# Optimization experiments

Measured on AMD Instinct MI355X. Metric: run time of the kernel, lower is better.

The kernel has to match this reference:

```python
import jax, jax.numpy as jnp
import numpy as np

V, E, H = 50000, 100, 128
B, S = 16, 4096
NUM_LEVELS = int(np.log2(S)) + 1  # 13; level l has S >> l nodes
# gate order in the 5-gate stack: i, f_l, f_r, o, u
XMAP = jnp.array([0, 1, 1, 2, 3])


def setup_inputs() -> dict:
    key = jax.random.key(0)
    ks = jax.random.split(key, 9)
    sE = 1.0 / np.sqrt(E)
    sH = 1.0 / np.sqrt(H)
    return {
        "embedding": jax.random.normal(ks[0], (V, E), jnp.float32) * 0.1,
        "W_x": jax.random.normal(ks[1], (4, H, E), jnp.float32) * sE,   # (i,f,o,u) x-projections
        "b_x": jax.random.normal(ks[2], (4, H), jnp.float32) * sE,
        "U_l": jax.random.normal(ks[3], (5, H, H), jnp.float32) * sH,   # (u_i_l,u_f_ll,u_f_rr,u_o_l,u_u_l) applied to h_left
        "b_l": jax.random.normal(ks[4], (5, H), jnp.float32) * sH,
        "U_r": jax.random.normal(ks[5], (5, H, H), jnp.float32) * sH,   # (u_i_r,u_f_lr,u_f_rl,u_o_r,u_u_r) applied to h_right
        "b_r": jax.random.normal(ks[6], (5, H), jnp.float32) * sH,
        "input_seq": jax.random.randint(ks[7], (B, S), 0, V, jnp.int32),
        "dep_tags": jax.random.randint(ks[8], (NUM_LEVELS - 1, S // 2), 0, S, jnp.int32),
    }


def _level_step(x5, h_l, h_r, c_l, c_r, U_l, b_l, U_r, b_r):
    # x5: [B,N,5,H] per-gate x contributions (w_*(x) incl. bias)
    pre = (x5
           + jnp.einsum('bnk,ghk->bngh', h_l, U_l) + b_l
           + jnp.einsum('bnk,ghk->bngh', h_r, U_r) + b_r)  # [B,N,5,H]
    i   = jax.nn.sigmoid(pre[:, :, 0])
    f_l = jax.nn.sigmoid(pre[:, :, 1])
    f_r = jax.nn.sigmoid(pre[:, :, 2])
    o   = jax.nn.sigmoid(pre[:, :, 3])
    u   = jnp.tanh(pre[:, :, 4])
    c = i * u + f_l * c_l + f_r * c_r
    h = o * jnp.tanh(c)
    return h, c


def reference(embedding, W_x, b_x, U_l, b_l, U_r, b_r, input_seq, dep_tags):
    b, s = input_seq.shape
    emb = embedding[input_seq]  # [B,S,E]
    xg = jnp.einsum('bse,ghe->bsgh', emb, W_x) + b_x  # [B,S,4,H]

    # level 0: every leaf is a token, children are zero
    z = jnp.zeros((b, s, xg.shape[-1]), xg.dtype)
    h, c = _level_step(xg[:, :, XMAP, :], z, z, z, z, U_l, b_l, U_r, b_r)

    for l in range(1, NUM_LEVELS):
        n = s >> l
        dep = dep_tags[l - 1, :n]                # token position re-embedded at each internal node
        x5 = xg[:, dep][:, :, XMAP, :]           # [B,N,5,H]
        hp = h.reshape(b, n, 2, -1)              # node i's children are (2i, 2i+1)
        cp = c.reshape(b, n, 2, -1)
        h, c = _level_step(x5, hp[:, :, 0], hp[:, :, 1], cp[:, :, 0], cp[:, :, 1],
                           U_l, b_l, U_r, b_r)
    return h[:, 0], c[:, 0]  # root (h, c): [B,H] each
```

## Files before the change

### kernel.cpp

```cpp
#include <hip/hip_runtime.h>
#include <hip/hip_bf16.h>

#define V_ 50000
#define E_ 100
#define H_ 128
#define B_ 16
#define S_ 4096

typedef unsigned short u16;
typedef unsigned int   u32;
typedef short bf16x8 __attribute__((ext_vector_type(8)));
typedef float f32x4  __attribute__((ext_vector_type(4)));

__device__ __forceinline__ float bf2f(u16 x) {
  return __uint_as_float(((u32)x) << 16);
}
__device__ __forceinline__ u16 f2bf(float x) {
  __hip_bfloat16 b = __float2bfloat16(x);
  return *reinterpret_cast<u16*>(&b);
}
__device__ __forceinline__ float sigm(float x) { return 1.0f / (1.0f + __expf(-x)); }
__device__ __forceinline__ float tanh_f(float x) {
  float e = __expf(2.0f * x);
  return 1.0f - 2.0f / (e + 1.0f);
}

#define PREP_N0 (V_ * 128)
#define PREP_N1 65536
#define PREP_N2 163840
#define PREP_N3 640
__global__ __launch_bounds__(256) void prep_all(
    const float* __restrict__ emb, const float* __restrict__ Wx,
    const float* __restrict__ Ul, const float* __restrict__ Ur,
    const float* __restrict__ bl, const float* __restrict__ br,
    u16* __restrict__ embB, u16* __restrict__ Bx, u16* __restrict__ Bu,
    float* __restrict__ bs)
{
  int i = blockIdx.x * 256 + threadIdx.x;
  if (i < PREP_N0) {
    int k = i & 127, t = i >> 7;
    embB[i] = (k < E_) ? f2bf(emb[t * E_ + k]) : (u16)0;
    return;
  }
  i -= PREP_N0;
  if (i < PREP_N1) {
    int j = i & 7, l = (i >> 3) & 63, s = (i >> 9) & 3, t = i >> 11;
    int k = s * 32 + (l >> 4) * 8 + j;
    int o = t * 16 + (l & 15);
    Bx[i] = (k < E_) ? f2bf(Wx[o * E_ + k]) : (u16)0;
    return;
  }
  i -= PREP_N1;
  if (i < PREP_N2) {
    int j = i & 7, l = (i >> 3) & 63, s = (i >> 9) & 7, t = i >> 12;
    int k = s * 32 + (l >> 4) * 8 + j;
    int gh = t * 16 + (l & 15);
    float v = (k < 128) ? Ul[gh * 128 + k] : Ur[gh * 128 + (k - 128)];
    Bu[i] = f2bf(v);
    return;
  }
  i -= PREP_N2;
  if (i < PREP_N3) bs[i] = bl[i] + br[i];
}

#define XLDS 516
__global__ __launch_bounds__(512) void xg_mfma(
    const u16* __restrict__ embB, const u16* __restrict__ Bx,
    const float* __restrict__ bx, const int* __restrict__ seq,
    const float* __restrict__ bs,
    ushort4* __restrict__ xg, u16* __restrict__ h0, float* __restrict__ c0)
{
  __shared__ u16 lds[32 * XLDS];
  const int w = threadIdx.x >> 6, lane = threadIdx.x & 63;
  const int quad = lane >> 4, l15 = lane & 15;
  const int m0 = blockIdx.x * 32;

  f32x4 acc[2][4];
  #pragma unroll
  for (int r = 0; r < 2; ++r)
    #pragma unroll
    for (int t = 0; t < 4; ++t) acc[r][t] = (f32x4){0.f, 0.f, 0.f, 0.f};

  int tok0 = seq[m0 + l15];
  int tok1 = seq[m0 + 16 + l15];
  const u16* a0p = embB + (size_t)tok0 * 128 + quad * 8;
  const u16* a1p = embB + (size_t)tok1 * 128 + quad * 8;

  #pragma unroll
  for (int s = 0; s < 4; ++s) {
    bf16x8 a0 = *reinterpret_cast<const bf16x8*>(a0p + s * 32);
    bf16x8 a1 = *reinterpret_cast<const bf16x8*>(a1p + s * 32);
    #pragma unroll
    for (int ti = 0; ti < 4; ++ti) {
      int t = w * 4 + ti;
      bf16x8 b = *reinterpret_cast<const bf16x8*>(Bx + ((size_t)(t * 4 + s) * 64 + lane) * 8);
      acc[0][ti] = __builtin_amdgcn_mfma_f32_16x16x32_bf16(a0, b, acc[0][ti], 0, 0, 0);
      acc[1][ti] = __builtin_amdgcn_mfma_f32_16x16x32_bf16(a1, b, acc[1][ti], 0, 0, 0);
    }
  }

  const int g = w >> 1;
  #pragma unroll
  for (int ti = 0; ti < 4; ++ti) {
    int o = (w * 4 + ti) * 16 + l15;
    float bxo = bx[o];
    int hhw = (w & 1) * 64 + ti * 16 + l15;
    #pragma unroll
    for (int r = 0; r < 2; ++r)
      #pragma unroll
      for (int reg = 0; reg < 4; ++reg) {
        int mrow = r * 16 + quad * 4 + reg;
        lds[mrow * XLDS + hhw * 4 + g] = f2bf(acc[r][ti][reg] + bxo);
      }
  }
  __syncthreads();

  #pragma unroll
  for (int i = 0; i < 8; ++i) {
    int pidx = i * 512 + threadIdx.x;
    int m = pidx >> 7, hh = pidx & 127;
    ushort4 v = *reinterpret_cast<const ushort4*>(&lds[m * XLDS + hh * 4]);
    size_t gm = (size_t)(m0 + m);
    xg[gm * 128 + hh] = v;
    float pi = bf2f(v.x) + bs[hh];
    float po = bf2f(v.z) + bs[384 + hh];
    float pu = bf2f(v.w) + bs[512 + hh];
    float c = sigm(pi) * tanh_f(pu);
    float h = sigm(po) * tanh_f(c);
    h0[gm * 128 + hh] = f2bf(h);
    c0[gm * 128 + hh] = c;
  }
}

__global__ __launch_bounds__(512) void level_mfma64(
    const ushort4* __restrict__ xg4, const int* __restrict__ deprow,
    const u16* __restrict__ Bu, const float* __restrict__ bs,
    const u16* __restrict__ hPrev, const float* __restrict__ cPrev,
    u16* __restrict__ hOut, float* __restrict__ cOut, int n, int ln2n)
{
  const int w = threadIdx.x >> 6, lane = threadIdx.x & 63;
  const int quad = lane >> 4, l15 = lane & 15;
  const int hh = w * 16 + l15;
  const int m0 = blockIdx.x * 64;

  ushort4 xv[16];
  #pragma unroll
  for (int i = 0; i < 16; ++i) {
    int m = m0 + (i >> 2) * 16 + quad * 4 + (i & 3);
    int j = m & (n - 1);
    int b = m >> ln2n;
    xv[i] = xg4[((size_t)b * S_ + deprow[j]) * 128 + hh];
  }

  f32x4 acc[4][5];
  #pragma unroll
  for (int r = 0; r < 4; ++r)
    #pragma unroll
    for (int g = 0; g < 5; ++g) acc[r][g] = (f32x4){0.f, 0.f, 0.f, 0.f};

  const u16* ap = hPrev + (size_t)(m0 + l15) * 256 + quad * 8;

  #pragma unroll
  for (int s = 0; s < 8; ++s) {
    bf16x8 a[4];
    #pragma unroll
    for (int r = 0; r < 4; ++r)
      a[r] = *reinterpret_cast<const bf16x8*>(ap + (size_t)r * 16 * 256 + s * 32);
    #pragma unroll
    for (int g = 0; g < 5; ++g) {
      int t = g * 8 + w;
      bf16x8 b = *reinterpret_cast<const bf16x8*>(Bu + ((size_t)(t * 8 + s) * 64 + lane) * 8);
      #pragma unroll
      for (int r = 0; r < 4; ++r)
        acc[r][g] = __builtin_amdgcn_mfma_f32_16x16x32_bf16(a[r], b, acc[r][g], 0, 0, 0);
    }
  }

  float bsv[5];
  #pragma unroll
  for (int g = 0; g < 5; ++g) bsv[g] = bs[g * 128 + hh];

  #pragma unroll
  for (int i = 0; i < 16; ++i) {
    int r = i >> 2, reg = i & 3;
    int m = m0 + r * 16 + quad * 4 + reg;
    ushort4 v = xv[i];
    float x0 = bf2f(v.x), x1 = bf2f(v.y), x2 = bf2f(v.z), x3 = bf2f(v.w);
    float cl = cPrev[(size_t)m * 256 + hh];
    float cr = cPrev[(size_t)m * 256 + 128 + hh];
    float pi  = acc[r][0][reg] + x0 + bsv[0];
    float pfl = acc[r][1][reg] + x1 + bsv[1];
    float pfr = acc[r][2][reg] + x1 + bsv[2];
    float po  = acc[r][3][reg] + x2 + bsv[3];
    float pu  = acc[r][4][reg] + x3 + bsv[4];
    float c = sigm(pi) * tanh_f(pu) + sigm(pfl) * cl + sigm(pfr) * cr;
    float h = sigm(po) * tanh_f(c);
    hOut[(size_t)m * 128 + hh] = f2bf(h);
    cOut[(size_t)m * 128 + hh] = c;
  }
}

__global__ __launch_bounds__(512) void level_mfma(
    const ushort4* __restrict__ xg4, const int* __restrict__ deprow,
    const u16* __restrict__ Bu, const float* __restrict__ bs,
    const u16* __restrict__ hPrev, const float* __restrict__ cPrev,
    u16* __restrict__ hOut, float* __restrict__ cOut, int n, int ln2n)
{
  const int w = threadIdx.x >> 6, lane = threadIdx.x & 63;
  const int quad = lane >> 4, l15 = lane & 15;
  const int hh = w * 16 + l15;
  const int m0 = blockIdx.x * 32;

  ushort4 xv[8];
  float clv[8], crv[8];
  #pragma unroll
  for (int i = 0; i < 8; ++i) {
    int m = m0 + (i >> 2) * 16 + quad * 4 + (i & 3);
    int j = m & (n - 1);
    int b = m >> ln2n;
    int dj = deprow[j];
    xv[i] = xg4[((size_t)b * S_ + dj) * 128 + hh];
    clv[i] = cPrev[(size_t)m * 256 + hh];
    crv[i] = cPrev[(size_t)m * 256 + 128 + hh];
  }

  f32x4 acc[2][5];
  #pragma unroll
  for (int r = 0; r < 2; ++r)
    #pragma unroll
    for (int g = 0; g < 5; ++g) acc[r][g] = (f32x4){0.f, 0.f, 0.f, 0.f};

  const u16* a0p = hPrev + (size_t)(m0 + l15) * 256 + quad * 8;
  const u16* a1p = a0p + 16 * 256;

  #pragma unroll
  for (int s = 0; s < 8; ++s) {
    bf16x8 a0 = *reinterpret_cast<const bf16x8*>(a0p + s * 32);
    bf16x8 a1 = *reinterpret_cast<const bf16x8*>(a1p + s * 32);
    #pragma unroll
    for (int g = 0; g < 5; ++g) {
      int t = g * 8 + w;
      bf16x8 b = *reinterpret_cast<const bf16x8*>(Bu + ((size_t)(t * 8 + s) * 64 + lane) * 8);
      acc[0][g] = __builtin_amdgcn_mfma_f32_16x16x32_bf16(a0, b, acc[0][g], 0, 0, 0);
      acc[1][g] = __builtin_amdgcn_mfma_f32_16x16x32_bf16(a1, b, acc[1][g], 0, 0, 0);
    }
  }

  float bsv[5];
  #pragma unroll
  for (int g = 0; g < 5; ++g) bsv[g] = bs[g * 128 + hh];

  #pragma unroll
  for (int i = 0; i < 8; ++i) {
    int r = i >> 2, reg = i & 3;
    int m = m0 + r * 16 + quad * 4 + reg;
    ushort4 v = xv[i];
    float x0 = bf2f(v.x), x1 = bf2f(v.y), x2 = bf2f(v.z), x3 = bf2f(v.w);
    float pi  = acc[r][0][reg] + x0 + bsv[0];
    float pfl = acc[r][1][reg] + x1 + bsv[1];
    float pfr = acc[r][2][reg] + x1 + bsv[2];
    float po  = acc[r][3][reg] + x2 + bsv[3];
    float pu  = acc[r][4][reg] + x3 + bsv[4];
    float c = sigm(pi) * tanh_f(pu) + sigm(pfl) * clv[i] + sigm(pfr) * crv[i];
    float h = sigm(po) * tanh_f(c);
    hOut[(size_t)m * 128 + hh] = f2bf(h);
    cOut[(size_t)m * 128 + hh] = c;
  }
}

__global__ __launch_bounds__(512) void deep_fused(
    const ushort4* __restrict__ xg4, const int* __restrict__ dep,
    const u16* __restrict__ Bu, const float* __restrict__ bs,
    const u16* __restrict__ h6, const float* __restrict__ c6,
    float* __restrict__ out)
{
  __shared__ u16  hls[2][32 * 136];
  __shared__ float cls[2][32 * 128];
  const int b = blockIdx.x;
  const int w = threadIdx.x >> 6, lane = threadIdx.x & 63;
  const int quad = lane >> 4, l15 = lane & 15;
  const int hh = w * 16 + l15;

  float bsv[5];
  #pragma unroll
  for (int g = 0; g < 5; ++g) bsv[g] = bs[g * 128 + hh];

  {
    ushort4 xv[2][4];
    float clv[2][4], crv[2][4];
    #pragma unroll
    for (int r = 0; r < 2; ++r)
      #pragma unroll
      for (int reg = 0; reg < 4; ++reg) {
        int j = r * 16 + quad * 4 + reg;
        int dj = dep[6 * 2048 + j];
        xv[r][reg] = xg4[((size_t)b * S_ + dj) * 128 + hh];
        clv[r][reg] = c6[(size_t)(b * 32 + j) * 256 + hh];
        crv[r][reg] = c6[(size_t)(b * 32 + j) * 256 + 128 + hh];
      }

    f32x4 acc[2][5];
    #pragma unroll
    for (int r = 0; r < 2; ++r)
      #pragma unroll
      for (int g = 0; g < 5; ++g) acc[r][g] = (f32x4){0.f, 0.f, 0.f, 0.f};

    #pragma unroll
    for (int s = 0; s < 8; ++s) {
      const u16* ap = h6 + (size_t)(b * 32 + l15) * 256 + s * 32 + quad * 8;
      bf16x8 a0 = *reinterpret_cast<const bf16x8*>(ap);
      bf16x8 a1 = *reinterpret_cast<const bf16x8*>(ap + 16 * 256);
      #pragma unroll
      for (int g = 0; g < 5; ++g) {
        int t = g * 8 + w;
        bf16x8 bb = *reinterpret_cast<const bf16x8*>(Bu + ((size_t)(t * 8 + s) * 64 + lane) * 8);
        acc[0][g] = __builtin_amdgcn_mfma_f32_16x16x32_bf16(a0, bb, acc[0][g], 0, 0, 0);
        acc[1][g] = __builtin_amdgcn_mfma_f32_16x16x32_bf16(a1, bb, acc[1][g], 0, 0, 0);
      }
    }

    #pragma unroll
    for (int r = 0; r < 2; ++r)
      #pragma unroll
      for (int reg = 0; reg < 4; ++reg) {
        int j = r * 16 + quad * 4 + reg;
        ushort4 v = xv[r][reg];
        float x0 = bf2f(v.x), x1 = bf2f(v.y), x2 = bf2f(v.z), x3 = bf2f(v.w);
        float pi  = acc[r][0][reg] + x0 + bsv[0];
        float pfl = acc[r][1][reg] + x1 + bsv[1];
        float pfr = acc[r][2][reg] + x1 + bsv[2];
        float po  = acc[r][3][reg] + x2 + bsv[3];
        float pu  = acc[r][4][reg] + x3 + bsv[4];
        float c = sigm(pi) * tanh_f(pu) + sigm(pfl) * clv[r][reg] + sigm(pfr) * crv[r][reg];
        float h = sigm(po) * tanh_f(c);
        hls[0][j * 136 + hh] = f2bf(h);
        cls[0][j * 128 + hh] = c;
      }
  }
  __syncthreads();

  ushort4 xvc[4];
  #pragma unroll
  for (int reg = 0; reg < 4; ++reg)
    xvc[reg] = xg4[((size_t)b * S_ + dep[7 * 2048 + quad * 4 + reg]) * 128 + hh];

  int pb = 0;
  for (int lvl = 8; lvl <= 12; ++lvl) {
    int nb = 4096 >> lvl;

    ushort4 xvn[4];
    if (lvl < 12) {
      int nbn = 2048 >> lvl;
      #pragma unroll
      for (int reg = 0; reg < 4; ++reg) {
        int j = quad * 4 + reg;
        if (j < nbn)
          xvn[reg] = xg4[((size_t)b * S_ + dep[lvl * 2048 + j]) * 128 + hh];
      }
    }

    f32x4 acc[5];
    #pragma unroll
    for (int g = 0; g < 5; ++g) acc[g] = (f32x4){0.f, 0.f, 0.f, 0.f};

    #pragma unroll
    for (int s = 0; s < 8; ++s) {
      int child = 2 * l15 + (s >= 4 ? 1 : 0);
      int kk = (s & 3) * 32 + quad * 8;
      bf16x8 a = *reinterpret_cast<const bf16x8*>(&hls[pb][child * 136 + kk]);
      #pragma unroll
      for (int g = 0; g < 5; ++g) {
        int t = g * 8 + w;
        bf16x8 bb = *reinterpret_cast<const bf16x8*>(Bu + ((size_t)(t * 8 + s) * 64 + lane) * 8);
        acc[g] = __builtin_amdgcn_mfma_f32_16x16x32_bf16(a, bb, acc[g], 0, 0, 0);
      }
    }

    #pragma unroll
    for (int reg = 0; reg < 4; ++reg) {
      int j = quad * 4 + reg;
      if (j < nb) {
        ushort4 v = xvc[reg];
        float x0 = bf2f(v.x), x1 = bf2f(v.y), x2 = bf2f(v.z), x3 = bf2f(v.w);
        float cl = cls[pb][(2 * j) * 128 + hh];
        float cr = cls[pb][(2 * j + 1) * 128 + hh];
        float pi  = acc[0][reg] + x0 + bsv[0];
        float pfl = acc[1][reg] + x1 + bsv[1];
        float pfr = acc[2][reg] + x1 + bsv[2];
        float po  = acc[3][reg] + x2 + bsv[3];
        float pu  = acc[4][reg] + x3 + bsv[4];
        float c = sigm(pi) * tanh_f(pu) + sigm(pfl) * cl + sigm(pfr) * cr;
        float h = sigm(po) * tanh_f(c);
        hls[pb ^ 1][j * 136 + hh] = f2bf(h);
        cls[pb ^ 1][j * 128 + hh] = c;
        if (lvl == 12) {
          out[b * 128 + hh] = h;
          out[2048 + b * 128 + hh] = c;
        }
      }
    }
    __syncthreads();
    pb ^= 1;
    #pragma unroll
    for (int reg = 0; reg < 4; ++reg) xvc[reg] = xvn[reg];
  }
}

extern "C" void kernel_launch(void* const* d_in, const int* in_sizes, int n_in,
                              void* d_out, int out_size, void* d_ws, size_t ws_size,
                              hipStream_t stream)
{
  const float* emb = (const float*)d_in[0];
  const float* Wx  = (const float*)d_in[1];
  const float* bx  = (const float*)d_in[2];
  const float* Ul  = (const float*)d_in[3];
  const float* bl  = (const float*)d_in[4];
  const float* Ur  = (const float*)d_in[5];
  const float* br  = (const float*)d_in[6];
  const int* seq = (const int*)d_in[7];
  const int* dep = (const int*)d_in[8];

  char* p = (char*)d_ws;
  u16* embB = (u16*)p;   p += (size_t)V_ * 128 * 2;
  u16* BswX = (u16*)p;   p += 131072;
  u16* BswU = (u16*)p;   p += 327680;
  float* bs = (float*)p; p += 4096;
  u16* xg = (u16*)p;     p += (size_t)B_ * S_ * 512 * 2;
  u16* hA = (u16*)p;     p += (size_t)B_ * S_ * H_ * 2;
  float* cA = (float*)p; p += (size_t)B_ * S_ * H_ * 4;
  u16* hB = (u16*)p;     p += (size_t)B_ * (S_ / 2) * H_ * 2;
  float* cB = (float*)p; p += (size_t)B_ * (S_ / 2) * H_ * 4;

  const int prep_tot = PREP_N0 + PREP_N1 + PREP_N2 + PREP_N3;
  prep_all<<<dim3((prep_tot + 255) / 256), dim3(256), 0, stream>>>(
      emb, Wx, Ul, Ur, bl, br, embB, BswX, BswU, bs);

  xg_mfma<<<dim3(B_ * S_ / 32), dim3(512), 0, stream>>>(
      embB, BswX, bx, seq, bs, (ushort4*)xg, hA, cA);

  const ushort4* xg4 = (const ushort4*)xg;
  u16 *hp = hA, *ho = hB;
  float *cp = cA, *co = cB;
  for (int l = 1; l <= 3; ++l) {
    int n = S_ >> l;
    int Mtot = B_ * n;
    const int* deprow = dep + (size_t)(l - 1) * (S_ / 2);
    level_mfma64<<<dim3(Mtot / 64), dim3(512), 0, stream>>>(
        xg4, deprow, BswU, bs, hp, cp, ho, co, n, 12 - l);
    u16* th = hp; hp = ho; ho = th;
    float* tc = cp; cp = co; co = tc;
  }
  for (int l = 4; l <= 6; ++l) {
    int n = S_ >> l;
    int Mtot = B_ * n;
    const int* deprow = dep + (size_t)(l - 1) * (S_ / 2);
    level_mfma<<<dim3(Mtot / 32), dim3(512), 0, stream>>>(
        xg4, deprow, BswU, bs, hp, cp, ho, co, n, 12 - l);
    u16* th = hp; hp = ho; ho = th;
    float* tc = cp; cp = co; co = tc;
  }

  deep_fused<<<dim3(16), dim3(512), 0, stream>>>(
      xg4, dep, BswU, bs, hp, cp, (float*)d_out);
}
```

Baseline: 271.0 us.

## Fuse level-0 leaf cell into level-1 kernel and fold biases into xg

```diff
diff --git a/kernel.cpp b/kernel.cpp
--- a/kernel.cpp
+++ b/kernel.cpp
@@ -33,8 +33,9 @@
     const float* __restrict__ emb, const float* __restrict__ Wx,
     const float* __restrict__ Ul, const float* __restrict__ Ur,
     const float* __restrict__ bl, const float* __restrict__ br,
+    const float* __restrict__ bx,
     u16* __restrict__ embB, u16* __restrict__ Bx, u16* __restrict__ Bu,
-    float* __restrict__ bs)
+    float* __restrict__ bxs, float* __restrict__ bd)
 {
   int i = blockIdx.x * 256 + threadIdx.x;
   if (i < PREP_N0) {
@@ -60,15 +61,21 @@
     return;
   }
   i -= PREP_N2;
-  if (i < PREP_N3) bs[i] = bl[i] + br[i];
-}
-
-#define XLDS 516
+  if (i < 512) {
+    int g = i >> 7, hh = i & 127;
+    int lg = (g == 0) ? 0 : (g == 1) ? 1 : (g == 2) ? 3 : 4;
+    bxs[i] = bx[i] + bl[lg * 128 + hh] + br[lg * 128 + hh];
+    return;
+  }
+  i -= 512;
+  if (i < 128) bd[i] = (bl[256 + i] + br[256 + i]) - (bl[128 + i] + br[128 + i]);
+}
+
+#define XLDS 514
 __global__ __launch_bounds__(512) void xg_mfma(
     const u16* __restrict__ embB, const u16* __restrict__ Bx,
-    const float* __restrict__ bx, const int* __restrict__ seq,
-    const float* __restrict__ bs,
-    ushort4* __restrict__ xg, u16* __restrict__ h0, float* __restrict__ c0)
+    const float* __restrict__ bxs, const int* __restrict__ seq,
+    ushort4* __restrict__ xg)
 {
   __shared__ u16 lds[32 * XLDS];
   const int w = threadIdx.x >> 6, lane = threadIdx.x & 63;
@@ -103,7 +110,7 @@
   #pragma unroll
   for (int ti = 0; ti < 4; ++ti) {
     int o = (w * 4 + ti) * 16 + l15;
-    float bxo = bx[o];
+    float bxo = bxs[o];
     int hhw = (w & 1) * 64 + ti * 16 + l15;
     #pragma unroll
     for (int r = 0; r < 2; ++r)
@@ -120,21 +127,97 @@
     int pidx = i * 512 + threadIdx.x;
     int m = pidx >> 7, hh = pidx & 127;
     ushort4 v = *reinterpret_cast<const ushort4*>(&lds[m * XLDS + hh * 4]);
-    size_t gm = (size_t)(m0 + m);
-    xg[gm * 128 + hh] = v;
-    float pi = bf2f(v.x) + bs[hh];
-    float po = bf2f(v.z) + bs[384 + hh];
-    float pu = bf2f(v.w) + bs[512 + hh];
-    float c = sigm(pi) * tanh_f(pu);
+    xg[(size_t)(m0 + m) * 128 + hh] = v;
+  }
+}
+
+__global__ __launch_bounds__(512) void level1_mfma(
+    const ushort4* __restrict__ xg4, const int* __restrict__ deprow,
+    const u16* __restrict__ Bu, const float* __restrict__ bd,
+    u16* __restrict__ hOut, float* __restrict__ cOut)
+{
+  const int w = threadIdx.x >> 6, lane = threadIdx.x & 63;
+  const int quad = lane >> 4, l15 = lane & 15;
+  const int hh = w * 16 + l15;
+  const int m0 = blockIdx.x * 32;
+
+  ushort4 xv[8];
+  #pragma unroll
+  for (int i = 0; i < 8; ++i) {
+    int m = m0 + (i >> 2) * 16 + quad * 4 + (i & 3);
+    int j = m & 2047;
+    int b = m >> 11;
+    xv[i] = xg4[((size_t)b * S_ + deprow[j]) * 128 + hh];
+  }
+
+  f32x4 acc[2][5];
+  #pragma unroll
+  for (int r = 0; r < 2; ++r)
+    #pragma unroll
+    for (int g = 0; g < 5; ++g) acc[r][g] = (f32x4){0.f, 0.f, 0.f, 0.f};
+
+  #pragma unroll
+  for (int s = 0; s < 8; ++s) {
+    bf16x8 a[2];
+    #pragma unroll
+    for (int r = 0; r < 2; ++r) {
+      int row2 = 2 * (m0 + r * 16 + l15) + (s >> 2);
+      const uint4* xp = reinterpret_cast<const uint4*>(
+          xg4 + (size_t)row2 * 128 + (s & 3) * 32 + quad * 8);
+      #pragma unroll
+      for (int jj = 0; jj < 4; ++jj) {
+        uint4 q = xp[jj];
+        {
+          float pi = __uint_as_float(q.x << 16);
+          float po = __uint_as_float(q.y << 16);
+          float pu = __uint_as_float(q.y & 0xffff0000u);
+          float c = sigm(pi) * tanh_f(pu);
+          a[r][2 * jj] = (short)f2bf(sigm(po) * tanh_f(c));
+        }
+        {
+          float pi = __uint_as_float(q.z << 16);
+          float po = __uint_as_float(q.w << 16);
+          float pu = __uint_as_float(q.w & 0xffff0000u);
+          float c = sigm(pi) * tanh_f(pu);
+          a[r][2 * jj + 1] = (short)f2bf(sigm(po) * tanh_f(c));
+        }
+      }
+    }
+    #pragma unroll
+    for (int g = 0; g < 5; ++g) {
+      int t = g * 8 + w;
+      bf16x8 b = *reinterpret_cast<const bf16x8*>(Bu + ((size_t)(t * 8 + s) * 64 + lane) * 8);
+      acc[0][g] = __builtin_amdgcn_mfma_f32_16x16x32_bf16(a[0], b, acc[0][g], 0, 0, 0);
+      acc[1][g] = __builtin_amdgcn_mfma_f32_16x16x32_bf16(a[1], b, acc[1][g], 0, 0, 0);
+    }
+  }
+
+  float bdv = bd[hh];
+  #pragma unroll
+  for (int i = 0; i < 8; ++i) {
+    int r = i >> 2, reg = i & 3;
+    int m = m0 + r * 16 + quad * 4 + reg;
+    ushort4 vl = xg4[(size_t)(2 * m) * 128 + hh];
+    ushort4 vr = xg4[(size_t)(2 * m + 1) * 128 + hh];
+    float cl = sigm(bf2f(vl.x)) * tanh_f(bf2f(vl.w));
+    float cr = sigm(bf2f(vr.x)) * tanh_f(bf2f(vr.w));
+    ushort4 v = xv[i];
+    float x0 = bf2f(v.x), x1 = bf2f(v.y), x2 = bf2f(v.z), x3 = bf2f(v.w);
+    float pi  = acc[r][0][reg] + x0;
+    float pfl = acc[r][1][reg] + x1;
+    float pfr = acc[r][2][reg] + x1 + bdv;
+    float po  = acc[r][3][reg] + x2;
+    float pu  = acc[r][4][reg] + x3;
+    float c = sigm(pi) * tanh_f(pu) + sigm(pfl) * cl + sigm(pfr) * cr;
     float h = sigm(po) * tanh_f(c);
-    h0[gm * 128 + hh] = f2bf(h);
-    c0[gm * 128 + hh] = c;
+    hOut[(size_t)m * 128 + hh] = f2bf(h);
+    cOut[(size_t)m * 128 + hh] = c;
   }
 }
 
 __global__ __launch_bounds__(512) void level_mfma64(
     const ushort4* __restrict__ xg4, const int* __restrict__ deprow,
-    const u16* __restrict__ Bu, const float* __restrict__ bs,
+    const u16* __restrict__ Bu, const float* __restrict__ bd,
     const u16* __restrict__ hPrev, const float* __restrict__ cPrev,
     u16* __restrict__ hOut, float* __restrict__ cOut, int n, int ln2n)
 {
@@ -176,10 +259,7 @@
     }
   }
 
-  float bsv[5];
-  #pragma unroll
-  for (int g = 0; g < 5; ++g) bsv[g] = bs[g * 128 + hh];
-
+  float bdv = bd[hh];
   #pragma unroll
   for (int i = 0; i < 16; ++i) {
     int r = i >> 2, reg = i & 3;
@@ -188,11 +268,11 @@
     float x0 = bf2f(v.x), x1 = bf2f(v.y), x2 = bf2f(v.z), x3 = bf2f(v.w);
     float cl = cPrev[(size_t)m * 256 + hh];
     float cr = cPrev[(size_t)m * 256 + 128 + hh];
-    float pi  = acc[r][0][reg] + x0 + bsv[0];
-    float pfl = acc[r][1][reg] + x1 + bsv[1];
-    float pfr = acc[r][2][reg] + x1 + bsv[2];
-    float po  = acc[r][3][reg] + x2 + bsv[3];
-    float pu  = acc[r][4][reg] + x3 + bsv[4];
+    float pi  = acc[r][0][reg] + x0;
+    float pfl = acc[r][1][reg] + x1;
+    float pfr = acc[r][2][reg] + x1 + bdv;
+    float po  = acc[r][3][reg] + x2;
+    float pu  = acc[r][4][reg] + x3;
     float c = sigm(pi) * tanh_f(pu) + sigm(pfl) * cl + sigm(pfr) * cr;
     float h = sigm(po) * tanh_f(c);
     hOut[(size_t)m * 128 + hh] = f2bf(h);
@@ -202,7 +282,7 @@
 
 __global__ __launch_bounds__(512) void level_mfma(
     const ushort4* __restrict__ xg4, const int* __restrict__ deprow,
-    const u16* __restrict__ Bu, const float* __restrict__ bs,
+    const u16* __restrict__ Bu, const float* __restrict__ bd,
     const u16* __restrict__ hPrev, const float* __restrict__ cPrev,
     u16* __restrict__ hOut, float* __restrict__ cOut, int n, int ln2n)
 {
@@ -246,21 +326,18 @@
     }
   }
 
-  float bsv[5];
-  #pragma unroll
-  for (int g = 0; g < 5; ++g) bsv[g] = bs[g * 128 + hh];
-
+  float bdv = bd[hh];
   #pragma unroll
   for (int i = 0; i < 8; ++i) {
     int r = i >> 2, reg = i & 3;
     int m = m0 + r * 16 + quad * 4 + reg;
     ushort4 v = xv[i];
     float x0 = bf2f(v.x), x1 = bf2f(v.y), x2 = bf2f(v.z), x3 = bf2f(v.w);
-    float pi  = acc[r][0][reg] + x0 + bsv[0];
-    float pfl = acc[r][1][reg] + x1 + bsv[1];
-    float pfr = acc[r][2][reg] + x1 + bsv[2];
-    float po  = acc[r][3][reg] + x2 + bsv[3];
-    float pu  = acc[r][4][reg] + x3 + bsv[4];
+    float pi  = acc[r][0][reg] + x0;
+    float pfl = acc[r][1][reg] + x1;
+    float pfr = acc[r][2][reg] + x1 + bdv;
+    float po  = acc[r][3][reg] + x2;
+    float pu  = acc[r][4][reg] + x3;
     float c = sigm(pi) * tanh_f(pu) + sigm(pfl) * clv[i] + sigm(pfr) * crv[i];
     float h = sigm(po) * tanh_f(c);
     hOut[(size_t)m * 128 + hh] = f2bf(h);
@@ -270,7 +347,7 @@
 
 __global__ __launch_bounds__(512) void deep_fused(
     const ushort4* __restrict__ xg4, const int* __restrict__ dep,
-    const u16* __restrict__ Bu, const float* __restrict__ bs,
+    const u16* __restrict__ Bu, const float* __restrict__ bd,
     const u16* __restrict__ h6, const float* __restrict__ c6,
     float* __restrict__ out)
 {
@@ -281,9 +358,7 @@
   const int quad = lane >> 4, l15 = lane & 15;
   const int hh = w * 16 + l15;
 
-  float bsv[5];
-  #pragma unroll
-  for (int g = 0; g < 5; ++g) bsv[g] = bs[g * 128 + hh];
+  const float bdv = bd[hh];
 
   {
     ushort4 xv[2][4];
@@ -326,11 +401,11 @@
         int j = r * 16 + quad * 4 + reg;
         ushort4 v = xv[r][reg];
         float x0 = bf2f(v.x), x1 = bf2f(v.y), x2 = bf2f(v.z), x3 = bf2f(v.w);
-        float pi  = acc[r][0][reg] + x0 + bsv[0];
-        float pfl = acc[r][1][reg] + x1 + bsv[1];
-        float pfr = acc[r][2][reg] + x1 + bsv[2];
-        float po  = acc[r][3][reg] + x2 + bsv[3];
-        float pu  = acc[r][4][reg] + x3 + bsv[4];
+        float pi  = acc[r][0][reg] + x0;
+        float pfl = acc[r][1][reg] + x1;
+        float pfr = acc[r][2][reg] + x1 + bdv;
+        float po  = acc[r][3][reg] + x2;
+        float pu  = acc[r][4][reg] + x3;
         float c = sigm(pi) * tanh_f(pu) + sigm(pfl) * clv[r][reg] + sigm(pfr) * crv[r][reg];
         float h = sigm(po) * tanh_f(c);
         hls[0][j * 136 + hh] = f2bf(h);
@@ -384,11 +459,11 @@
         float x0 = bf2f(v.x), x1 = bf2f(v.y), x2 = bf2f(v.z), x3 = bf2f(v.w);
         float cl = cls[pb][(2 * j) * 128 + hh];
         float cr = cls[pb][(2 * j + 1) * 128 + hh];
-        float pi  = acc[0][reg] + x0 + bsv[0];
-        float pfl = acc[1][reg] + x1 + bsv[1];
-        float pfr = acc[2][reg] + x1 + bsv[2];
-        float po  = acc[3][reg] + x2 + bsv[3];
-        float pu  = acc[4][reg] + x3 + bsv[4];
+        float pi  = acc[0][reg] + x0;
+        float pfl = acc[1][reg] + x1;
+        float pfr = acc[2][reg] + x1 + bdv;
+        float po  = acc[3][reg] + x2;
+        float pu  = acc[4][reg] + x3;
         float c = sigm(pi) * tanh_f(pu) + sigm(pfl) * cl + sigm(pfr) * cr;
         float h = sigm(po) * tanh_f(c);
         hls[pb ^ 1][j * 136 + hh] = f2bf(h);
@@ -424,29 +499,34 @@
   u16* embB = (u16*)p;   p += (size_t)V_ * 128 * 2;
   u16* BswX = (u16*)p;   p += 131072;
   u16* BswU = (u16*)p;   p += 327680;
-  float* bs = (float*)p; p += 4096;
+  float* bxs = (float*)p; p += 2048;
+  float* bd = (float*)p;  p += 2048;
   u16* xg = (u16*)p;     p += (size_t)B_ * S_ * 512 * 2;
-  u16* hA = (u16*)p;     p += (size_t)B_ * S_ * H_ * 2;
-  float* cA = (float*)p; p += (size_t)B_ * S_ * H_ * 4;
-  u16* hB = (u16*)p;     p += (size_t)B_ * (S_ / 2) * H_ * 2;
-  float* cB = (float*)p; p += (size_t)B_ * (S_ / 2) * H_ * 4;
+  u16* hA = (u16*)p;     p += (size_t)32768 * 128 * 2;
+  float* cA = (float*)p; p += (size_t)32768 * 128 * 4;
+  u16* hB = (u16*)p;     p += (size_t)16384 * 128 * 2;
+  float* cB = (float*)p; p += (size_t)16384 * 128 * 4;
 
   const int prep_tot = PREP_N0 + PREP_N1 + PREP_N2 + PREP_N3;
   prep_all<<<dim3((prep_tot + 255) / 256), dim3(256), 0, stream>>>(
-      emb, Wx, Ul, Ur, bl, br, embB, BswX, BswU, bs);
+      emb, Wx, Ul, Ur, bl, br, bx, embB, BswX, BswU, bxs, bd);
 
   xg_mfma<<<dim3(B_ * S_ / 32), dim3(512), 0, stream>>>(
-      embB, BswX, bx, seq, bs, (ushort4*)xg, hA, cA);
+      embB, BswX, bxs, seq, (ushort4*)xg);
 
   const ushort4* xg4 = (const ushort4*)xg;
+
+  level1_mfma<<<dim3(1024), dim3(512), 0, stream>>>(
+      xg4, dep, BswU, bd, hA, cA);
+
   u16 *hp = hA, *ho = hB;
   float *cp = cA, *co = cB;
-  for (int l = 1; l <= 3; ++l) {
+  for (int l = 2; l <= 3; ++l) {
     int n = S_ >> l;
     int Mtot = B_ * n;
     const int* deprow = dep + (size_t)(l - 1) * (S_ / 2);
     level_mfma64<<<dim3(Mtot / 64), dim3(512), 0, stream>>>(
-        xg4, deprow, BswU, bs, hp, cp, ho, co, n, 12 - l);
+        xg4, deprow, BswU, bd, hp, cp, ho, co, n, 12 - l);
     u16* th = hp; hp = ho; ho = th;
     float* tc = cp; cp = co; co = tc;
   }
@@ -455,11 +535,11 @@
     int Mtot = B_ * n;
     const int* deprow = dep + (size_t)(l - 1) * (S_ / 2);
     level_mfma<<<dim3(Mtot / 32), dim3(512), 0, stream>>>(
-        xg4, deprow, BswU, bs, hp, cp, ho, co, n, 12 - l);
+        xg4, deprow, BswU, bd, hp, cp, ho, co, n, 12 - l);
     u16* th = hp; hp = ho; ho = th;
     float* tc = cp; cp = co; co = tc;
   }
 
   deep_fused<<<dim3(16), dim3(512), 0, stream>>>(
-      xg4, dep, BswU, bs, hp, cp, (float*)d_out);
-}
+      xg4, dep, BswU, bd, hp, cp, (float*)d_out);
+}
```

After: 372.8 us. 1.38x slower.
